# Optimization experiments

Measured on AMD Instinct MI355X. Metric: run time of the kernel, lower is better.

The kernel has to match this reference:

```python
import jax, jax.numpy as jnp
import numpy as np

NS, NT, DF, H, O = 200000, 50000, 20, 64, 64
NE, NL = 1000000, 500000


def setup_inputs() -> dict:
    key = jax.random.key(0)
    ks = jax.random.split(key, 24)
    inp = {
        'target_x': jax.random.normal(ks[0], (NT, DF), jnp.float32),
        'source_node_id': jnp.arange(NS, dtype=jnp.int64),
        'target_node_id': jnp.arange(NT, dtype=jnp.int64),
        'edge_src': jax.random.randint(ks[1], (NE,), 0, NS),
        'edge_dst': jax.random.randint(ks[2], (NE,), 0, NT),
        'label_src': jax.random.randint(ks[3], (NL,), 0, NS),
        'label_dst': jax.random.randint(ks[4], (NL,), 0, NT),
        'src_emb': jax.random.normal(ks[5], (NS, H), jnp.float32) * 0.05,
        'tgt_emb': jax.random.normal(ks[6], (NT, H), jnp.float32) * 0.05,
        'lin_W': jax.random.normal(ks[7], (DF, H), jnp.float32) * 0.05,
        'lin_b': jnp.zeros((H,), jnp.float32),
    }
    # SAGEConv params: (Wl, bl, Wr) per edge type per layer. st = source->target, ts = target->source
    dims = {'st1': (H, H), 'ts1': (H, H), 'st2': (H, O), 'ts2': (H, O)}
    i = 8
    for name, (din, dout) in dims.items():
        inp['Wl_' + name] = jax.random.normal(ks[i], (din, dout), jnp.float32) * 0.05
        inp['bl_' + name] = jnp.zeros((dout,), jnp.float32)
        inp['Wr_' + name] = jax.random.normal(ks[i + 1], (din, dout), jnp.float32) * 0.05
        i += 2
    return inp


def _sage(x_src, x_dst, src_idx, dst_idx, n_dst, Wl, bl, Wr):
    # PyG SAGEConv, aggr='mean': lin_l(mean_{j in N(i)} x_j) + lin_r(x_i)
    msg = x_src[src_idx]                                   # [E, d] gather
    agg = jax.ops.segment_sum(msg, dst_idx, num_segments=n_dst)
    deg = jax.ops.segment_sum(jnp.ones((src_idx.shape[0],), x_src.dtype), dst_idx, num_segments=n_dst)
    mean = agg / jnp.maximum(deg, 1.0)[:, None]
    return mean @ Wl + bl + x_dst @ Wr


def reference(target_x, source_node_id, target_node_id, edge_src, edge_dst,
              label_src, label_dst, src_emb, tgt_emb, lin_W, lin_b,
              Wl_st1, bl_st1, Wr_st1, Wl_ts1, bl_ts1, Wr_ts1,
              Wl_st2, bl_st2, Wr_st2, Wl_ts2, bl_ts2, Wr_ts2):
    ns, nt = src_emb.shape[0], tgt_emb.shape[0]
    x_s = src_emb[source_node_id]                          # [NS, H]
    x_t = target_x @ lin_W + lin_b + tgt_emb[target_node_id]  # [NT, H]
    # layer 1 (per edge type, summed per dst type; each dst type has one incoming type)
    h_t = _sage(x_s, x_t, edge_src, edge_dst, nt, Wl_st1, bl_st1, Wr_st1)
    h_s = _sage(x_t, x_s, edge_dst, edge_src, ns, Wl_ts1, bl_ts1, Wr_ts1)
    h_t, h_s = jax.nn.relu(h_t), jax.nn.relu(h_s)
    # layer 2
    o_t = _sage(h_s, h_t, edge_src, edge_dst, nt, Wl_st2, bl_st2, Wr_st2)
    o_s = _sage(h_t, h_s, edge_dst, edge_src, ns, Wl_ts2, bl_ts2, Wr_ts2)
    # dot-product link classifier
    return (o_s[label_src] * o_t[label_dst]).sum(axis=-1)  # [NL]
```

## Files before the change

kernel.cpp:

```cpp
#include <hip/hip_runtime.h>

#define NSRC 200000
#define NTGT 50000
#define DF   20
#define HD   64
#define NE   1000000
#define NL   500000

#define SH_T 6
#define SH_S 8
#define NB   782
#define CHUNK 8192
#define NCH  ((NE + CHUNK - 1) / CHUNK)

#define HIST_BLKS (NCH * 2)
#define PREP_BLKS 256

#define GT 782
#define GS 3125

typedef unsigned short ushort_t;
typedef short s16x8 __attribute__((ext_vector_type(8)));
typedef float f32x4 __attribute__((ext_vector_type(4)));

__device__ __forceinline__ float bf2f(ushort_t u) {
    return __uint_as_float(((unsigned)u) << 16);
}
__device__ __forceinline__ ushort_t f2bf(float f) {
    unsigned u = __float_as_uint(f);
    return (ushort_t)((u + 0x7fffu + ((u >> 16) & 1u)) >> 16);
}

__global__ __launch_bounds__(1024) void front(
    const int* __restrict__ es, const int* __restrict__ ed,
    int* __restrict__ cnt_t, int* __restrict__ cnt_s,
    const float* __restrict__ tx, const float* __restrict__ W,
    const float* __restrict__ lb, const float* __restrict__ temb,
    const float* __restrict__ semb,
    ushort_t* __restrict__ xb, ushort_t* __restrict__ sbuf,
    const float* __restrict__ Wl0, const float* __restrict__ Wr0,
    const float* __restrict__ Wl1, const float* __restrict__ Wr1,
    const float* __restrict__ Wl2, const float* __restrict__ Wr2,
    const float* __restrict__ Wl3, const float* __restrict__ Wr3,
    ushort_t* __restrict__ wt)
{
    __shared__ int h[NB];
    const int b   = blockIdx.x;
    const int tid = threadIdx.x;

    if (b < HIST_BLKS) {
        const int dir  = b / NCH;
        const int c    = b % NCH;
        const int base = c * CHUNK;
        const int n    = min(CHUNK, NE - base);
        const int* key = dir ? es : ed;
        const int sh   = dir ? SH_S : SH_T;
        int* cnt       = dir ? cnt_s : cnt_t;

        for (int i = tid; i < NB; i += 1024) h[i] = 0;
        __syncthreads();
        for (int i = tid; i < n; i += 1024)
            atomicAdd(&h[key[base + i] >> sh], 1);
        __syncthreads();
        for (int i = tid; i < NB; i += 1024) cnt[c * NB + i] = h[i];
    } else if (b < HIST_BLKS + PREP_BLKS) {
        const int id   = (b - HIST_BLKS) * 1024 + tid;
        const int pstr = PREP_BLKS * 1024;
        for (int i = id; i < NTGT * HD; i += pstr) {
            int n = i >> 6, k = i & 63;
            float acc = lb[k] + temb[i];
#pragma unroll
            for (int d = 0; d < DF; ++d) acc += tx[n * DF + d] * W[d * HD + k];
            xb[i] = f2bf(acc);
        }
        for (int i = id; i < NSRC * HD; i += pstr) sbuf[i] = f2bf(semb[i]);
    } else {
        for (int i = tid; i < 4 * 64 * 128; i += 1024) {
            int set = i >> 13, rem = i & 8191;
            int j = rem >> 7, k = rem & 127;
            const float* Wl = set == 0 ? Wl0 : set == 1 ? Wl1 : set == 2 ? Wl2 : Wl3;
            const float* Wr = set == 0 ? Wr0 : set == 1 ? Wr1 : set == 2 ? Wr2 : Wr3;
            float v = (k < 64) ? Wl[k * 64 + j] : Wr[(k - 64) * 64 + j];
            wt[i] = f2bf(v);
        }
    }
}

__global__ __launch_bounds__(1024) void scan_all(
    int* __restrict__ cnt_t, int* __restrict__ cnt_s,
    int* __restrict__ bb_t, int* __restrict__ bb_s)
{
    int* cnt = blockIdx.x ? cnt_s : cnt_t;
    int* bb  = blockIdx.x ? bb_s  : bb_t;
    __shared__ int s[1024];
    const int tid = threadIdx.x;
    int run = 0;
    if (tid < NB) {
        for (int c = 0; c < NCH; ++c) {
            int v = cnt[c * NB + tid];
            cnt[c * NB + tid] = run;
            run += v;
        }
    }
    s[tid] = (tid < NB) ? run : 0;
    __syncthreads();
    for (int d = 1; d < 1024; d <<= 1) {
        int t = (tid >= d) ? s[tid - d] : 0;
        __syncthreads();
        s[tid] += t;
        __syncthreads();
    }
    int incl = s[tid];
    if (tid < NB) bb[tid] = incl - run;
    if (tid == NB - 1) bb[NB] = incl;
}

__global__ __launch_bounds__(1024) void bin_fill2(
    const int* __restrict__ es, const int* __restrict__ ed,
    const int* __restrict__ cnt_t, const int* __restrict__ cnt_s,
    const int* __restrict__ bb_t, const int* __restrict__ bb_s,
    int2* __restrict__ pairs_t, int2* __restrict__ pairs_s)
{
    __shared__ int cur[NB];
    const int dir  = blockIdx.y;
    const int c    = blockIdx.x;
    const int base = c * CHUNK;
    const int n    = min(CHUNK, NE - base);
    const int* key = dir ? es : ed;
    const int* oth = dir ? ed : es;
    const int sh   = dir ? SH_S : SH_T;
    const int* cnt = dir ? cnt_s : cnt_t;
    const int* bb  = dir ? bb_s  : bb_t;
    int2* pairs    = dir ? pairs_s : pairs_t;

    for (int i = threadIdx.x; i < NB; i += 1024)
        cur[i] = bb[i] + cnt[c * NB + i];
    __syncthreads();
    for (int i = threadIdx.x; i < n; i += 1024) {
        int k = key[base + i], o = oth[base + i];
        int p = atomicAdd(&cur[k >> sh], 1);
        pairs[p] = make_int2(o, k);
    }
}

__global__ __launch_bounds__(256) void bucket_build_all(
    const int2* __restrict__ pairs_t, const int* __restrict__ bb_t,
    int* __restrict__ rp_t, int* __restrict__ col_t,
    const int2* __restrict__ pairs_s, const int* __restrict__ bb_s,
    int* __restrict__ rp_s, int* __restrict__ col_s)
{
    __shared__ int hist[256];
    __shared__ int scn[256];
    __shared__ int cur[256];
    const bool is_t = blockIdx.x < NB;
    const int b = is_t ? blockIdx.x : blockIdx.x - NB;
    const int2* pairs = is_t ? pairs_t : pairs_s;
    const int* bb     = is_t ? bb_t : bb_s;
    int* rp           = is_t ? rp_t : rp_s;
    int* col          = is_t ? col_t : col_s;
    const int shift   = is_t ? SH_T : SH_S;
    const int n       = is_t ? NTGT : NSRC;

    const int tid = threadIdx.x;
    const int beg = bb[b], end = bb[b + 1];
    const int row0 = b << shift;

    hist[tid] = 0;
    __syncthreads();
    for (int e = beg + tid; e < end; e += 256)
        atomicAdd(&hist[pairs[e].y - row0], 1);
    __syncthreads();

    int v = hist[tid];
    scn[tid] = v;
    __syncthreads();
    for (int d = 1; d < 256; d <<= 1) {
        int t = (tid >= d) ? scn[tid - d] : 0;
        __syncthreads();
        scn[tid] += t;
        __syncthreads();
    }
    int ex = scn[tid] - v;
    cur[tid] = ex;
    int row = row0 + tid;
    if (tid < (1 << shift) && row < n) rp[row] = beg + ex;
    if (b == 0 && tid == 0) rp[n] = NE;
    __syncthreads();

    for (int e = beg + tid; e < end; e += 256) {
        int2 pr = pairs[e];
        int p = atomicAdd(&cur[pr.y - row0], 1);
        col[beg + p] = pr.x;
    }
}

template <bool RELU>
__global__ __launch_bounds__(256) void sage_layer(
    const ushort_t* __restrict__ tab_t, const int* __restrict__ rp_t,
    const int* __restrict__ col_t, const ushort_t* __restrict__ xd_t,
    const ushort_t* __restrict__ wt_t, const float* __restrict__ bl_t,
    ushort_t* __restrict__ out_t,
    const ushort_t* __restrict__ tab_s, const int* __restrict__ rp_s,
    const int* __restrict__ col_s, const ushort_t* __restrict__ xd_s,
    const ushort_t* __restrict__ wt_s, const float* __restrict__ bl_s,
    ushort_t* __restrict__ out_s)
{
    __shared__ ushort_t smean[64][72];
    const int blk = blockIdx.x;
    const bool is_t = (blk % 5 == 0);
    const int bi = is_t ? blk / 5 : blk - blk / 5 - 1;

    const ushort_t* table = is_t ? tab_t : tab_s;
    const int* rp         = is_t ? rp_t  : rp_s;
    const int* col        = is_t ? col_t : col_s;
    const ushort_t* xd    = is_t ? xd_t  : xd_s;
    const ushort_t* wt    = is_t ? wt_t  : wt_s;
    const float* bl       = is_t ? bl_t  : bl_s;
    ushort_t* out         = is_t ? out_t : out_s;
    const int n           = is_t ? NTGT  : NSRC;

    const int tid = threadIdx.x;
    const int el  = tid & 7;
    const int ew  = tid >> 3;
    const int d0  = el * 8;
    const int base = bi * 64;

    const int node0 = base + ew;
    const int node1 = base + ew + 32;
    int e0 = 0, end0 = 0, e1 = 0, end1 = 0;
    if (node0 < n) { e0 = rp[node0]; end0 = rp[node0 + 1]; }
    if (node1 < n) { e1 = rp[node1]; end1 = rp[node1 + 1]; }
    const float inv0 = (end0 > e0) ? 1.f / (float)(end0 - e0) : 0.f;
    const float inv1 = (end1 > e1) ? 1.f / (float)(end1 - e1) : 0.f;

    float r0[4][8], r1[4][8];
#pragma unroll
    for (int s = 0; s < 4; ++s)
#pragma unroll
        for (int i = 0; i < 8; ++i) { r0[s][i] = 0.f; r1[s][i] = 0.f; }

    while (e0 < end0 || e1 < end1) {
        const bool w0 = e0 < end0, w1 = e1 < end1;
        s16x8 v0[4], v1[4];
        if (w0) {
            int c[4];
#pragma unroll
            for (int s = 0; s < 4; ++s) c[s] = col[min(e0 + s, end0 - 1)];
#pragma unroll
            for (int s = 0; s < 4; ++s)
                v0[s] = *(const s16x8*)&table[(size_t)c[s] * HD + d0];
        }
        if (w1) {
            int c[4];
#pragma unroll
            for (int s = 0; s < 4; ++s) c[s] = col[min(e1 + s, end1 - 1)];
#pragma unroll
            for (int s = 0; s < 4; ++s)
                v1[s] = *(const s16x8*)&table[(size_t)c[s] * HD + d0];
        }
        if (w0) {
#pragma unroll
            for (int s = 0; s < 4; ++s)
                if (e0 + s < end0)
#pragma unroll
                    for (int i = 0; i < 8; ++i) r0[s][i] += bf2f((ushort_t)v0[s][i]);
            e0 += 4;
        }
        if (w1) {
#pragma unroll
            for (int s = 0; s < 4; ++s)
                if (e1 + s < end1)
#pragma unroll
                    for (int i = 0; i < 8; ++i) r1[s][i] += bf2f((ushort_t)v1[s][i]);
            e1 += 4;
        }
    }

    s16x8 o0, o1;
#pragma unroll
    for (int i = 0; i < 8; ++i) {
        o0[i] = (short)f2bf((r0[0][i] + r0[1][i] + r0[2][i] + r0[3][i]) * inv0);
        o1[i] = (short)f2bf((r1[0][i] + r1[1][i] + r1[2][i] + r1[3][i]) * inv1);
    }
    *(s16x8*)&smean[ew][d0] = o0;
    *(s16x8*)&smean[ew + 32][d0] = o1;
    __syncthreads();

    const int lane = tid & 63;
    const int wid  = tid >> 6;
    const int lr   = lane & 15;
    const int kg   = lane >> 4;

    s16x8 bfr[4][4];
#pragma unroll
    for (int jb = 0; jb < 4; ++jb)
#pragma unroll
        for (int kb = 0; kb < 4; ++kb)
            bfr[jb][kb] = *(const s16x8*)&wt[(jb * 16 + lr) * 128 + kb * 32 + kg * 8];

    float bias[4];
#pragma unroll
    for (int jb = 0; jb < 4; ++jb) bias[jb] = bl[jb * 16 + lr];

    const int arow = base + wid * 16 + lr;
    s16x8 a[4];
    a[0] = *(const s16x8*)&smean[wid * 16 + lr][kg * 8];
    a[1] = *(const s16x8*)&smean[wid * 16 + lr][32 + kg * 8];
    if (arow < n) {
        const ushort_t* xrow = xd + (size_t)arow * HD;
        a[2] = *(const s16x8*)(xrow + kg * 8);
        a[3] = *(const s16x8*)(xrow + 32 + kg * 8);
    } else {
        s16x8 z = {0, 0, 0, 0, 0, 0, 0, 0};
        a[2] = z; a[3] = z;
    }

    const int drow0 = base + wid * 16 + kg * 4;
#pragma unroll
    for (int jb = 0; jb < 4; ++jb) {
        f32x4 acc = {bias[jb], bias[jb], bias[jb], bias[jb]};
#pragma unroll
        for (int kb = 0; kb < 4; ++kb)
            acc = __builtin_amdgcn_mfma_f32_16x16x32_bf16(a[kb], bfr[jb][kb], acc, 0, 0, 0);
#pragma unroll
        for (int r = 0; r < 4; ++r) {
            int nn = drow0 + r;
            if (nn < n) {
                float v = acc[r];
                if (RELU) v = fmaxf(v, 0.f);
                out[(size_t)nn * HD + jb * 16 + lr] = f2bf(v);
            }
        }
    }
}

__global__ __launch_bounds__(256) void classify_b(
    const ushort_t* __restrict__ os, const ushort_t* __restrict__ ot,
    const int* __restrict__ ls, const int* __restrict__ lt,
    float* __restrict__ out, int nl)
{
    const int lane = threadIdx.x & 63;
    const int sub  = lane >> 4;
    const int g    = (lane & 15) * 4;
    int w = (blockIdx.x * blockDim.x + threadIdx.x) >> 6;
    const int wstride = (gridDim.x * blockDim.x) >> 6;

    for (int l0 = w * 8; l0 < nl; l0 += wstride * 8) {
        int la = l0 + sub;
        int lb = l0 + 4 + sub;
        float pa = 0.f, pb = 0.f;
        if (la < nl) {
            int a = ls[la], b = lt[la];
            ushort4 va = *(const ushort4*)&os[(size_t)a * HD + g];
            ushort4 vb = *(const ushort4*)&ot[(size_t)b * HD + g];
            pa = bf2f(va.x) * bf2f(vb.x) + bf2f(va.y) * bf2f(vb.y)
               + bf2f(va.z) * bf2f(vb.z) + bf2f(va.w) * bf2f(vb.w);
        }
        if (lb < nl) {
            int a = ls[lb], b = lt[lb];
            ushort4 va = *(const ushort4*)&os[(size_t)a * HD + g];
            ushort4 vb = *(const ushort4*)&ot[(size_t)b * HD + g];
            pb = bf2f(va.x) * bf2f(vb.x) + bf2f(va.y) * bf2f(vb.y)
               + bf2f(va.z) * bf2f(vb.z) + bf2f(va.w) * bf2f(vb.w);
        }
#pragma unroll
        for (int o = 8; o > 0; o >>= 1) {
            pa += __shfl_xor(pa, o, 64);
            pb += __shfl_xor(pb, o, 64);
        }
        if ((lane & 15) == 0) {
            if (la < nl) out[la] = pa;
            if (lb < nl) out[lb] = pb;
        }
    }
}

extern "C" void kernel_launch(void* const* d_in, const int* in_sizes, int n_in,
                              void* d_out, int out_size, void* d_ws, size_t ws_size,
                              hipStream_t stream)
{
    const float* target_x = (const float*)d_in[0];
    const int* edge_src  = (const int*)d_in[3];
    const int* edge_dst  = (const int*)d_in[4];
    const int* label_src = (const int*)d_in[5];
    const int* label_dst = (const int*)d_in[6];
    const float* src_emb = (const float*)d_in[7];
    const float* tgt_emb = (const float*)d_in[8];
    const float* lin_W   = (const float*)d_in[9];
    const float* lin_b   = (const float*)d_in[10];
    const float* Wl_st1 = (const float*)d_in[11];
    const float* bl_st1 = (const float*)d_in[12];
    const float* Wr_st1 = (const float*)d_in[13];
    const float* Wl_ts1 = (const float*)d_in[14];
    const float* bl_ts1 = (const float*)d_in[15];
    const float* Wr_ts1 = (const float*)d_in[16];
    const float* Wl_st2 = (const float*)d_in[17];
    const float* bl_st2 = (const float*)d_in[18];
    const float* Wr_st2 = (const float*)d_in[19];
    const float* Wl_ts2 = (const float*)d_in[20];
    const float* bl_ts2 = (const float*)d_in[21];
    const float* Wr_ts2 = (const float*)d_in[22];
    float* out = (float*)d_out;

    char* ws = (char*)d_ws;
    size_t off = 0;
    auto take = [&](size_t bytes) -> char* {
        char* p = ws + off;
        off = (off + bytes + 255) & ~(size_t)255;
        return p;
    };
    int* cnt_t = (int*)take((size_t)NCH * NB * 4);
    int* cnt_s = (int*)take((size_t)NCH * NB * 4);
    int* bb_t  = (int*)take((size_t)(NB + 1) * 4);
    int* bb_s  = (int*)take((size_t)(NB + 1) * 4);
    int* rp_t  = (int*)take((size_t)(NTGT + 1) * 4);
    int* rp_s  = (int*)take((size_t)(NSRC + 1) * 4);
    int* col_t = (int*)take((size_t)NE * 4);
    int* col_s = (int*)take((size_t)NE * 4);
    int2* pairs_t = (int2*)take((size_t)NE * 8);
    int2* pairs_s = (int2*)take((size_t)NE * 8);
    ushort_t* wt   = (ushort_t*)take((size_t)4 * 64 * 128 * 2);
    ushort_t* xb_t = (ushort_t*)take((size_t)NTGT * HD * 2);
    ushort_t* sb   = (ushort_t*)take((size_t)NSRC * HD * 2);
    ushort_t* hb_t = (ushort_t*)take((size_t)NTGT * HD * 2);
    ushort_t* hb_s = (ushort_t*)take((size_t)NSRC * HD * 2);
    ushort_t* ob_t = (ushort_t*)take((size_t)NTGT * HD * 2);
    ushort_t* ob_s = (ushort_t*)take((size_t)NSRC * HD * 2);

    front<<<HIST_BLKS + PREP_BLKS + 1, 1024, 0, stream>>>(
        edge_src, edge_dst, cnt_t, cnt_s,
        target_x, lin_W, lin_b, tgt_emb, src_emb, xb_t, sb,
        Wl_st1, Wr_st1, Wl_ts1, Wr_ts1, Wl_st2, Wr_st2, Wl_ts2, Wr_ts2, wt);

    scan_all<<<2, 1024, 0, stream>>>(cnt_t, cnt_s, bb_t, bb_s);
    dim3 gch(NCH, 2);
    bin_fill2<<<gch, 1024, 0, stream>>>(edge_src, edge_dst,
                                        cnt_t, cnt_s, bb_t, bb_s, pairs_t, pairs_s);
    bucket_build_all<<<2 * NB, 256, 0, stream>>>(pairs_t, bb_t, rp_t, col_t,
                                                 pairs_s, bb_s, rp_s, col_s);

    sage_layer<true><<<GT + GS, 256, 0, stream>>>(
        sb,   rp_t, col_t, xb_t, wt + 0 * 8192, bl_st1, hb_t,
        xb_t, rp_s, col_s, sb,   wt + 1 * 8192, bl_ts1, hb_s);
    sage_layer<false><<<GT + GS, 256, 0, stream>>>(
        hb_s, rp_t, col_t, hb_t, wt + 2 * 8192, bl_st2, ob_t,
        hb_t, rp_s, col_s, hb_s, wt + 3 * 8192, bl_ts2, ob_s);

    classify_b<<<2048, 256, 0, stream>>>(ob_s, ob_t, label_src, label_dst, out, NL);
}
```

Measured before the change: 277.8 us.

## Use 1024-thread SAGE blocks with one node per 16 lanes and per-wave MFMA tiles

The SAGE layer kernel now runs 1024 threads per block. Each 16-lane group gathers one destination node's neighbours using 4-element bf16 loads, unrolled 6 edges deep. Each of the 16 waves then computes one 16x16 MFMA output tile, where before each wave computed four. The aim is more memory-level parallelism in the irregular gather and less per-thread serial work on high-degree nodes, at the cost of narrower loads and more threads per block. The classify kernel is also unrolled to handle 4 label pairs per lane group per iteration instead of 2, so more loads are in flight.

```diff
diff --git a/kernel.cpp b/kernel.cpp
--- a/kernel.cpp
+++ b/kernel.cpp
@@ -195,7 +195,7 @@
 }
 
 template <bool RELU>
-__global__ __launch_bounds__(256) void sage_layer(
+__global__ __launch_bounds__(1024, 8) void sage_layer(
     const ushort_t* __restrict__ tab_t, const int* __restrict__ rp_t,
     const int* __restrict__ col_t, const ushort_t* __restrict__ xd_t,
     const ushort_t* __restrict__ wt_t, const float* __restrict__ bl_t,
@@ -220,92 +220,67 @@
     const int n           = is_t ? NTGT  : NSRC;
 
     const int tid = threadIdx.x;
-    const int el  = tid & 7;
-    const int ew  = tid >> 3;
-    const int d0  = el * 8;
+    const int ql  = tid & 15;
+    const int qw  = tid >> 4;
+    const int d0  = ql * 4;
     const int base = bi * 64;
 
-    const int node0 = base + ew;
-    const int node1 = base + ew + 32;
-    int e0 = 0, end0 = 0, e1 = 0, end1 = 0;
-    if (node0 < n) { e0 = rp[node0]; end0 = rp[node0 + 1]; }
-    if (node1 < n) { e1 = rp[node1]; end1 = rp[node1 + 1]; }
-    const float inv0 = (end0 > e0) ? 1.f / (float)(end0 - e0) : 0.f;
-    const float inv1 = (end1 > e1) ? 1.f / (float)(end1 - e1) : 0.f;
-
-    float r0[4][8], r1[4][8];
-#pragma unroll
-    for (int s = 0; s < 4; ++s)
-#pragma unroll
-        for (int i = 0; i < 8; ++i) { r0[s][i] = 0.f; r1[s][i] = 0.f; }
-
-    while (e0 < end0 || e1 < end1) {
-        const bool w0 = e0 < end0, w1 = e1 < end1;
-        s16x8 v0[4], v1[4];
-        if (w0) {
-            int c[4];
-#pragma unroll
-            for (int s = 0; s < 4; ++s) c[s] = col[min(e0 + s, end0 - 1)];
-#pragma unroll
-            for (int s = 0; s < 4; ++s)
-                v0[s] = *(const s16x8*)&table[(size_t)c[s] * HD + d0];
-        }
-        if (w1) {
-            int c[4];
-#pragma unroll
-            for (int s = 0; s < 4; ++s) c[s] = col[min(e1 + s, end1 - 1)];
-#pragma unroll
-            for (int s = 0; s < 4; ++s)
-                v1[s] = *(const s16x8*)&table[(size_t)c[s] * HD + d0];
-        }
-        if (w0) {
-#pragma unroll
-            for (int s = 0; s < 4; ++s)
-                if (e0 + s < end0)
-#pragma unroll
-                    for (int i = 0; i < 8; ++i) r0[s][i] += bf2f((ushort_t)v0[s][i]);
-            e0 += 4;
-        }
-        if (w1) {
-#pragma unroll
-            for (int s = 0; s < 4; ++s)
-                if (e1 + s < end1)
-#pragma unroll
-                    for (int i = 0; i < 8; ++i) r1[s][i] += bf2f((ushort_t)v1[s][i]);
-            e1 += 4;
-        }
-    }
-
-    s16x8 o0, o1;
-#pragma unroll
-    for (int i = 0; i < 8; ++i) {
-        o0[i] = (short)f2bf((r0[0][i] + r0[1][i] + r0[2][i] + r0[3][i]) * inv0);
-        o1[i] = (short)f2bf((r1[0][i] + r1[1][i] + r1[2][i] + r1[3][i]) * inv1);
-    }
-    *(s16x8*)&smean[ew][d0] = o0;
-    *(s16x8*)&smean[ew + 32][d0] = o1;
+    const int node = base + qw;
+    int e = 0, end = 0;
+    if (node < n) { e = rp[node]; end = rp[node + 1]; }
+    const float inv = (end > e) ? 1.f / (float)(end - e) : 0.f;
+
+    float acc[6][4];
+#pragma unroll
+    for (int s = 0; s < 6; ++s)
+#pragma unroll
+        for (int i = 0; i < 4; ++i) acc[s][i] = 0.f;
+
+    while (e < end) {
+        ushort4 v[6];
+#pragma unroll
+        for (int s = 0; s < 6; ++s)
+            if (e + s < end) {
+                int c = col[e + s];
+                v[s] = *(const ushort4*)&table[(size_t)c * HD + d0];
+            }
+#pragma unroll
+        for (int s = 0; s < 6; ++s)
+            if (e + s < end) {
+                acc[s][0] += bf2f(v[s].x);
+                acc[s][1] += bf2f(v[s].y);
+                acc[s][2] += bf2f(v[s].z);
+                acc[s][3] += bf2f(v[s].w);
+            }
+        e += 6;
+    }
+
+    ushort4 o;
+    o.x = f2bf((acc[0][0] + acc[1][0] + acc[2][0] + acc[3][0] + acc[4][0] + acc[5][0]) * inv);
+    o.y = f2bf((acc[0][1] + acc[1][1] + acc[2][1] + acc[3][1] + acc[4][1] + acc[5][1]) * inv);
+    o.z = f2bf((acc[0][2] + acc[1][2] + acc[2][2] + acc[3][2] + acc[4][2] + acc[5][2]) * inv);
+    o.w = f2bf((acc[0][3] + acc[1][3] + acc[2][3] + acc[3][3] + acc[4][3] + acc[5][3]) * inv);
+    *(ushort4*)&smean[qw][d0] = o;
     __syncthreads();
 
     const int lane = tid & 63;
     const int wid  = tid >> 6;
+    const int rq   = wid & 3;
+    const int jb   = wid >> 2;
     const int lr   = lane & 15;
     const int kg   = lane >> 4;
 
-    s16x8 bfr[4][4];
-#pragma unroll
-    for (int jb = 0; jb < 4; ++jb)
-#pragma unroll
-        for (int kb = 0; kb < 4; ++kb)
-            bfr[jb][kb] = *(const s16x8*)&wt[(jb * 16 + lr) * 128 + kb * 32 + kg * 8];
-
-    float bias[4];
-#pragma unroll
-    for (int jb = 0; jb < 4; ++jb) bias[jb] = bl[jb * 16 + lr];
-
-    const int arow = base + wid * 16 + lr;
+    s16x8 bfr[4];
+#pragma unroll
+    for (int kb = 0; kb < 4; ++kb)
+        bfr[kb] = *(const s16x8*)&wt[(jb * 16 + lr) * 128 + kb * 32 + kg * 8];
+
+    const float bias = bl[jb * 16 + lr];
+
+    const int arow = base + rq * 16 + lr;
     s16x8 a[4];
-    a[0] = *(const s16x8*)&smean[wid * 16 + lr][kg * 8];
-    a[1] = *(const s16x8*)&smean[wid * 16 + lr][32 + kg * 8];
+    a[0] = *(const s16x8*)&smean[rq * 16 + lr][kg * 8];
+    a[1] = *(const s16x8*)&smean[rq * 16 + lr][32 + kg * 8];
     if (arow < n) {
         const ushort_t* xrow = xd + (size_t)arow * HD;
         a[2] = *(const s16x8*)(xrow + kg * 8);
@@ -315,21 +290,19 @@
         a[2] = z; a[3] = z;
     }
 
-    const int drow0 = base + wid * 16 + kg * 4;
-#pragma unroll
-    for (int jb = 0; jb < 4; ++jb) {
-        f32x4 acc = {bias[jb], bias[jb], bias[jb], bias[jb]};
-#pragma unroll
-        for (int kb = 0; kb < 4; ++kb)
-            acc = __builtin_amdgcn_mfma_f32_16x16x32_bf16(a[kb], bfr[jb][kb], acc, 0, 0, 0);
-#pragma unroll
-        for (int r = 0; r < 4; ++r) {
-            int nn = drow0 + r;
-            if (nn < n) {
-                float v = acc[r];
-                if (RELU) v = fmaxf(v, 0.f);
-                out[(size_t)nn * HD + jb * 16 + lr] = f2bf(v);
-            }
+    f32x4 accm = {bias, bias, bias, bias};
+#pragma unroll
+    for (int kb = 0; kb < 4; ++kb)
+        accm = __builtin_amdgcn_mfma_f32_16x16x32_bf16(a[kb], bfr[kb], accm, 0, 0, 0);
+
+    const int drow0 = base + rq * 16 + kg * 4;
+#pragma unroll
+    for (int r = 0; r < 4; ++r) {
+        int nn = drow0 + r;
+        if (nn < n) {
+            float v = accm[r];
+            if (RELU) v = fmaxf(v, 0.f);
+            out[(size_t)nn * HD + jb * 16 + lr] = f2bf(v);
         }
     }
 }
@@ -345,32 +318,29 @@
     int w = (blockIdx.x * blockDim.x + threadIdx.x) >> 6;
     const int wstride = (gridDim.x * blockDim.x) >> 6;
 
-    for (int l0 = w * 8; l0 < nl; l0 += wstride * 8) {
-        int la = l0 + sub;
-        int lb = l0 + 4 + sub;
-        float pa = 0.f, pb = 0.f;
-        if (la < nl) {
-            int a = ls[la], b = lt[la];
-            ushort4 va = *(const ushort4*)&os[(size_t)a * HD + g];
-            ushort4 vb = *(const ushort4*)&ot[(size_t)b * HD + g];
-            pa = bf2f(va.x) * bf2f(vb.x) + bf2f(va.y) * bf2f(vb.y)
-               + bf2f(va.z) * bf2f(vb.z) + bf2f(va.w) * bf2f(vb.w);
-        }
-        if (lb < nl) {
-            int a = ls[lb], b = lt[lb];
-            ushort4 va = *(const ushort4*)&os[(size_t)a * HD + g];
-            ushort4 vb = *(const ushort4*)&ot[(size_t)b * HD + g];
-            pb = bf2f(va.x) * bf2f(vb.x) + bf2f(va.y) * bf2f(vb.y)
-               + bf2f(va.z) * bf2f(vb.z) + bf2f(va.w) * bf2f(vb.w);
-        }
+    for (int l0 = w * 16; l0 < nl; l0 += wstride * 16) {
+        float p[4];
+        int li[4];
+#pragma unroll
+        for (int q = 0; q < 4; ++q) { li[q] = l0 + q * 4 + sub; p[q] = 0.f; }
+#pragma unroll
+        for (int q = 0; q < 4; ++q)
+            if (li[q] < nl) {
+                int a = ls[li[q]], b = lt[li[q]];
+                ushort4 va = *(const ushort4*)&os[(size_t)a * HD + g];
+                ushort4 vb = *(const ushort4*)&ot[(size_t)b * HD + g];
+                p[q] = bf2f(va.x) * bf2f(vb.x) + bf2f(va.y) * bf2f(vb.y)
+                     + bf2f(va.z) * bf2f(vb.z) + bf2f(va.w) * bf2f(vb.w);
+            }
 #pragma unroll
         for (int o = 8; o > 0; o >>= 1) {
-            pa += __shfl_xor(pa, o, 64);
-            pb += __shfl_xor(pb, o, 64);
+#pragma unroll
+            for (int q = 0; q < 4; ++q) p[q] += __shfl_xor(p[q], o, 64);
         }
         if ((lane & 15) == 0) {
-            if (la < nl) out[la] = pa;
-            if (lb < nl) out[lb] = pb;
+#pragma unroll
+            for (int q = 0; q < 4; ++q)
+                if (li[q] < nl) out[li[q]] = p[q];
         }
     }
 }
@@ -439,10 +409,10 @@
     bucket_build_all<<<2 * NB, 256, 0, stream>>>(pairs_t, bb_t, rp_t, col_t,
                                                  pairs_s, bb_s, rp_s, col_s);
 
-    sage_layer<true><<<GT + GS, 256, 0, stream>>>(
+    sage_layer<true><<<GT + GS, 1024, 0, stream>>>(
         sb,   rp_t, col_t, xb_t, wt + 0 * 8192, bl_st1, hb_t,
         xb_t, rp_s, col_s, sb,   wt + 1 * 8192, bl_ts1, hb_s);
-    sage_layer<false><<<GT + GS, 256, 0, stream>>>(
+    sage_layer<false><<<GT + GS, 1024, 0, stream>>>(
         hb_s, rp_t, col_t, hb_t, wt + 2 * 8192, bl_st2, ob_t,
         hb_t, rp_s, col_s, hb_s, wt + 3 * 8192, bl_ts2, ob_s);
 
```

New measurement: 333.6 us. 1.2x slower.

## Cut sage_layer register pressure for occupancy and widen classifier per-wave batching

Applied to the files above, without the earlier changes.

The sage_layer kernel now asks for 8 blocks per CU and uses a single accumulator per node instead of four partial sums. It also loads the weight fragments for each output column block inside a non-unrolled loop instead of keeping all 16 fragments resident. The aim is lower VGPR use and higher occupancy for the latency-bound gather. The classifier now processes 4 label pairs per lane group instead of 2, putting more loads in flight. Risks are a longer dependency chain on the single accumulator, repeated weight loads per block, and possible spills under the tighter launch bound.

```diff
diff --git a/kernel.cpp b/kernel.cpp
--- a/kernel.cpp
+++ b/kernel.cpp
@@ -195,7 +195,7 @@
 }
 
 template <bool RELU>
-__global__ __launch_bounds__(256) void sage_layer(
+__global__ __launch_bounds__(256, 8) void sage_layer(
     const ushort_t* __restrict__ tab_t, const int* __restrict__ rp_t,
     const int* __restrict__ col_t, const ushort_t* __restrict__ xd_t,
     const ushort_t* __restrict__ wt_t, const float* __restrict__ bl_t,
@@ -233,11 +233,9 @@
     const float inv0 = (end0 > e0) ? 1.f / (float)(end0 - e0) : 0.f;
     const float inv1 = (end1 > e1) ? 1.f / (float)(end1 - e1) : 0.f;
 
-    float r0[4][8], r1[4][8];
-#pragma unroll
-    for (int s = 0; s < 4; ++s)
-#pragma unroll
-        for (int i = 0; i < 8; ++i) { r0[s][i] = 0.f; r1[s][i] = 0.f; }
+    float r0[8], r1[8];
+#pragma unroll
+    for (int i = 0; i < 8; ++i) { r0[i] = 0.f; r1[i] = 0.f; }
 
     while (e0 < end0 || e1 < end1) {
         const bool w0 = e0 < end0, w1 = e1 < end1;
@@ -263,7 +261,7 @@
             for (int s = 0; s < 4; ++s)
                 if (e0 + s < end0)
 #pragma unroll
-                    for (int i = 0; i < 8; ++i) r0[s][i] += bf2f((ushort_t)v0[s][i]);
+                    for (int i = 0; i < 8; ++i) r0[i] += bf2f((ushort_t)v0[s][i]);
             e0 += 4;
         }
         if (w1) {
@@ -271,7 +269,7 @@
             for (int s = 0; s < 4; ++s)
                 if (e1 + s < end1)
 #pragma unroll
-                    for (int i = 0; i < 8; ++i) r1[s][i] += bf2f((ushort_t)v1[s][i]);
+                    for (int i = 0; i < 8; ++i) r1[i] += bf2f((ushort_t)v1[s][i]);
             e1 += 4;
         }
     }
@@ -279,33 +277,22 @@
     s16x8 o0, o1;
 #pragma unroll
     for (int i = 0; i < 8; ++i) {
-        o0[i] = (short)f2bf((r0[0][i] + r0[1][i] + r0[2][i] + r0[3][i]) * inv0);
-        o1[i] = (short)f2bf((r1[0][i] + r1[1][i] + r1[2][i] + r1[3][i]) * inv1);
+        o0[i] = (short)f2bf(r0[i] * inv0);
+        o1[i] = (short)f2bf(r1[i] * inv1);
     }
     *(s16x8*)&smean[ew][d0] = o0;
     *(s16x8*)&smean[ew + 32][d0] = o1;
     __syncthreads();
 
     const int lane = tid & 63;
-    const int wid  = tid >> 6;
+    const int rq   = tid >> 6;
     const int lr   = lane & 15;
     const int kg   = lane >> 4;
 
-    s16x8 bfr[4][4];
-#pragma unroll
-    for (int jb = 0; jb < 4; ++jb)
-#pragma unroll
-        for (int kb = 0; kb < 4; ++kb)
-            bfr[jb][kb] = *(const s16x8*)&wt[(jb * 16 + lr) * 128 + kb * 32 + kg * 8];
-
-    float bias[4];
-#pragma unroll
-    for (int jb = 0; jb < 4; ++jb) bias[jb] = bl[jb * 16 + lr];
-
-    const int arow = base + wid * 16 + lr;
+    const int arow = base + rq * 16 + lr;
     s16x8 a[4];
-    a[0] = *(const s16x8*)&smean[wid * 16 + lr][kg * 8];
-    a[1] = *(const s16x8*)&smean[wid * 16 + lr][32 + kg * 8];
+    a[0] = *(const s16x8*)&smean[rq * 16 + lr][kg * 8];
+    a[1] = *(const s16x8*)&smean[rq * 16 + lr][32 + kg * 8];
     if (arow < n) {
         const ushort_t* xrow = xd + (size_t)arow * HD;
         a[2] = *(const s16x8*)(xrow + kg * 8);
@@ -315,18 +302,25 @@
         a[2] = z; a[3] = z;
     }
 
-    const int drow0 = base + wid * 16 + kg * 4;
-#pragma unroll
+    const int drow0 = base + rq * 16 + kg * 4;
+#pragma unroll 1
     for (int jb = 0; jb < 4; ++jb) {
-        f32x4 acc = {bias[jb], bias[jb], bias[jb], bias[jb]};
+        s16x8 bfr[4];
 #pragma unroll
         for (int kb = 0; kb < 4; ++kb)
-            acc = __builtin_amdgcn_mfma_f32_16x16x32_bf16(a[kb], bfr[jb][kb], acc, 0, 0, 0);
+            bfr[kb] = *(const s16x8*)&wt[(jb * 16 + lr) * 128 + kb * 32 + kg * 8];
+        const float bias = bl[jb * 16 + lr];
+
+        f32x4 accm = {bias, bias, bias, bias};
+#pragma unroll
+        for (int kb = 0; kb < 4; ++kb)
+            accm = __builtin_amdgcn_mfma_f32_16x16x32_bf16(a[kb], bfr[kb], accm, 0, 0, 0);
+
 #pragma unroll
         for (int r = 0; r < 4; ++r) {
             int nn = drow0 + r;
             if (nn < n) {
-                float v = acc[r];
+                float v = accm[r];
                 if (RELU) v = fmaxf(v, 0.f);
                 out[(size_t)nn * HD + jb * 16 + lr] = f2bf(v);
             }
@@ -345,32 +339,29 @@
     int w = (blockIdx.x * blockDim.x + threadIdx.x) >> 6;
     const int wstride = (gridDim.x * blockDim.x) >> 6;
 
-    for (int l0 = w * 8; l0 < nl; l0 += wstride * 8) {
-        int la = l0 + sub;
-        int lb = l0 + 4 + sub;
-        float pa = 0.f, pb = 0.f;
-        if (la < nl) {
-            int a = ls[la], b = lt[la];
-            ushort4 va = *(const ushort4*)&os[(size_t)a * HD + g];
-            ushort4 vb = *(const ushort4*)&ot[(size_t)b * HD + g];
-            pa = bf2f(va.x) * bf2f(vb.x) + bf2f(va.y) * bf2f(vb.y)
-               + bf2f(va.z) * bf2f(vb.z) + bf2f(va.w) * bf2f(vb.w);
-        }
-        if (lb < nl) {
-            int a = ls[lb], b = lt[lb];
-            ushort4 va = *(const ushort4*)&os[(size_t)a * HD + g];
-            ushort4 vb = *(const ushort4*)&ot[(size_t)b * HD + g];
-            pb = bf2f(va.x) * bf2f(vb.x) + bf2f(va.y) * bf2f(vb.y)
-               + bf2f(va.z) * bf2f(vb.z) + bf2f(va.w) * bf2f(vb.w);
-        }
+    for (int l0 = w * 16; l0 < nl; l0 += wstride * 16) {
+        float p[4];
+        int li[4];
+#pragma unroll
+        for (int q = 0; q < 4; ++q) { li[q] = l0 + q * 4 + sub; p[q] = 0.f; }
+#pragma unroll
+        for (int q = 0; q < 4; ++q)
+            if (li[q] < nl) {
+                int a = ls[li[q]], b = lt[li[q]];
+                ushort4 va = *(const ushort4*)&os[(size_t)a * HD + g];
+                ushort4 vb = *(const ushort4*)&ot[(size_t)b * HD + g];
+                p[q] = bf2f(va.x) * bf2f(vb.x) + bf2f(va.y) * bf2f(vb.y)
+                     + bf2f(va.z) * bf2f(vb.z) + bf2f(va.w) * bf2f(vb.w);
+            }
 #pragma unroll
         for (int o = 8; o > 0; o >>= 1) {
-            pa += __shfl_xor(pa, o, 64);
-            pb += __shfl_xor(pb, o, 64);
+#pragma unroll
+            for (int q = 0; q < 4; ++q) p[q] += __shfl_xor(p[q], o, 64);
         }
         if ((lane & 15) == 0) {
-            if (la < nl) out[la] = pa;
-            if (lb < nl) out[lb] = pb;
+#pragma unroll
+            for (int q = 0; q < 4; ++q)
+                if (li[q] < nl) out[li[q]] = p[q];
         }
     }
 }
```

After: 273.7 us. About the same (-1.5%).
